# Optimization experiments

Hardware: AMD Instinct MI355X
Metric: run time of the kernel (lower is better)

The kernel has to match this reference:

```python
import jax, jax.numpy as jnp
import numpy as np
from jax import lax

H = W = 224
FH = FW = 7          # backbone feature map spatial size
THRESH = 0.7
NUM_CLASSES = 14


def _conv(x, w, stride, pad):
    return lax.conv_general_dilated(
        x, w, (stride, stride), [(pad, pad), (pad, pad)],
        dimension_numbers=('NCHW', 'OIHW', 'NCHW'))


def backbone(x, w0, w1, w2, w3, fw, fb):
    # stand-in resnet50 trunk: 224 -> 56 -> 28 -> 14 -> 7, channels 3->64->512->1024->2048
    h = jax.nn.relu(_conv(x, w0, 4, 3))      # [B,64,56,56]
    h = jax.nn.relu(_conv(h, w1, 2, 1))      # [B,512,28,28]
    h = jax.nn.relu(_conv(h, w2, 2, 1))      # [B,1024,14,14]
    feat = jax.nn.relu(_conv(h, w3, 2, 1))   # [B,2048,7,7]
    pool = feat.max(axis=(2, 3))             # MaxPool2d(k=7,s=1) on 7x7 == global max -> [B,2048]
    out = jax.nn.sigmoid(pool @ fw.T + fb)   # fc + Sigmoid -> [B,14]
    return out, feat, pool


def attention_gen_patchs(img, fm):
    B, C, Hh, Ww = img.shape
    # per-sample channel-max abs heatmap, min-max normalized
    hm = jnp.max(jnp.abs(fm), axis=1)                              # [B,7,7]
    mn = hm.min(axis=(1, 2), keepdims=True)
    mx = hm.max(axis=(1, 2), keepdims=True)
    hm = (hm - mn) / (mx - mn)
    hm = jax.image.resize(hm, (B, Hh, Ww), method='bilinear')      # Resize((h,w))
    mask = (hm > THRESH).astype(jnp.int32)                         # [B,H,W]

    # largest 8-connected component: iterative max-label propagation
    ids = jnp.arange(1, Hh * Ww + 1, dtype=jnp.int32).reshape(1, Hh, Ww) * mask
    def body(_, lab):
        p = lax.reduce_window(lab, jnp.int32(0), lax.max, (1, 3, 3), (1, 1, 1), 'SAME')
        return p * mask
    labels = lax.fori_loop(0, Hh + Ww, body, ids)                  # [B,H,W] int32

    def counts_one(lab):
        c = jnp.zeros((Hh * Ww + 1,), jnp.int32).at[lab.reshape(-1)].add(1)
        return c.at[0].set(-1)                                     # ignore background
    counts = jax.vmap(counts_one)(labels)                          # [B,H*W+1]
    max_label = jnp.argmax(counts, axis=1)                         # [B]
    lcc = labels == max_label[:, None, None]                       # [B,H,W] bool

    # bbox of largest component (xmin/xmax over rows, ymin/ymax over cols)
    ri = jnp.arange(Hh); ci = jnp.arange(Ww)
    rows = lcc.any(axis=2); cols = lcc.any(axis=1)
    xmin = jnp.min(jnp.where(rows, ri[None, :], Hh), axis=1)
    xmax = jnp.max(jnp.where(rows, ri[None, :], -1), axis=1)       # inclusive; torch slice excludes it
    ymin = jnp.min(jnp.where(cols, ci[None, :], Ww), axis=1)
    ymax = jnp.max(jnp.where(cols, ci[None, :], -1), axis=1)
    ch = jnp.maximum(xmax - xmin, 1).astype(jnp.float32)           # crop height (exclusive slice)
    cw = jnp.maximum(ymax - ymin, 1).astype(jnp.float32)

    # bilinear resize of crop [xmin:xmax, ymin:ymax] back to (H,W), align_corners=False
    fy0 = xmin.astype(jnp.float32); fx0 = ymin.astype(jnp.float32)
    oy = (jnp.arange(Hh, dtype=jnp.float32) + 0.5)[None, :] * (ch[:, None] / Hh) + fy0[:, None] - 0.5
    ox = (jnp.arange(Ww, dtype=jnp.float32) + 0.5)[None, :] * (cw[:, None] / Ww) + fx0[:, None] - 0.5
    oy = jnp.clip(oy, fy0[:, None], jnp.maximum(fy0 + ch - 1.0, fy0)[:, None])
    ox = jnp.clip(ox, fx0[:, None], jnp.maximum(fx0 + cw - 1.0, fx0)[:, None])

    def sample_one(im, yy, xx):  # im [C,H,W]
        gy = jnp.broadcast_to(yy[:, None], (Hh, Ww))
        gx = jnp.broadcast_to(xx[None, :], (Hh, Ww))
        f = lambda chan: jax.scipy.ndimage.map_coordinates(chan, [gy, gx], order=1, mode='nearest')
        return jax.vmap(f)(im)
    return jax.vmap(sample_one)(img, oy, ox)                       # [B,C,H,W]


def bce(p, t):
    p = jnp.clip(p, 1e-7, 1.0 - 1e-7)
    return -jnp.mean(t * jnp.log(p) + (1.0 - t) * jnp.log1p(-p))


def setup_inputs() -> dict:
    key = jax.random.key(0)
    ks = jax.random.split(key, 20)
    B = 4
    def conv_w(k, o, i, s):
        return jax.random.normal(k, (o, i, s, s), jnp.float32) * np.sqrt(2.0 / (i * s * s)).astype(np.float32)
    def lin(k, o, i):
        return jax.random.normal(k, (o, i), jnp.float32) * np.sqrt(1.0 / i).astype(np.float32)
    inp = {
        'img': jax.random.uniform(ks[0], (B, 3, H, W), jnp.float32),
        'target': jax.random.uniform(ks[1], (B, NUM_CLASSES), jnp.float32),
        'gw0': conv_w(ks[2], 64, 3, 7), 'gw1': conv_w(ks[3], 512, 64, 3),
        'gw2': conv_w(ks[4], 1024, 512, 3), 'gw3': conv_w(ks[5], 2048, 1024, 3),
        'gfw': lin(ks[6], NUM_CLASSES, 2048), 'gfb': jnp.zeros((NUM_CLASSES,), jnp.float32),
        'lw0': conv_w(ks[7], 64, 3, 7), 'lw1': conv_w(ks[8], 512, 64, 3),
        'lw2': conv_w(ks[9], 1024, 512, 3), 'lw3': conv_w(ks[10], 2048, 1024, 3),
        'lfw': lin(ks[11], NUM_CLASSES, 2048), 'lfb': jnp.zeros((NUM_CLASSES,), jnp.float32),
        'fw': lin(ks[12], NUM_CLASSES, 2048 * 2), 'fb': jnp.zeros((NUM_CLASSES,), jnp.float32),
    }
    return inp


def reference(img, target, gw0, gw1, gw2, gw3, gfw, gfb,
              lw0, lw1, lw2, lw3, lfw, lfb, fw, fb):
    out_g, fm_g, pool_g = backbone(img, gw0, gw1, gw2, gw3, gfw, gfb)
    # patch generation is non-differentiable in the original (CPU/PIL round trip)
    patch = attention_gen_patchs(lax.stop_gradient(img), lax.stop_gradient(fm_g))
    out_l, _, pool_l = backbone(patch, lw0, lw1, lw2, lw3, lfw, lfb)
    out_f = jax.nn.sigmoid(jnp.concatenate([pool_g, pool_l], axis=1) @ fw.T + fb)
    gl = bce(out_g, target); ll = bce(out_l, target); fl = bce(out_f, target)
    loss = 0.8 * gl + 0.1 * ll + 0.1 * fl
    return loss, out_g, out_l, out_f, patch
```

## Files before the change

kernel.cpp:

```cpp
#include <hip/hip_runtime.h>
#include <math.h>

typedef __attribute__((ext_vector_type(8))) short short8m;
typedef __attribute__((ext_vector_type(4))) float f32x4;

__device__ inline unsigned short bf16_trunc(float f) {
  return (unsigned short)(__float_as_uint(f) >> 16);
}
__device__ inline unsigned short bf16_rte(float f) {
  unsigned u = __float_as_uint(f);
  u += 0x7fffu + ((u >> 16) & 1u);
  return (unsigned short)(u >> 16);
}
__device__ inline float bf16_tof(unsigned short h) {
  return __uint_as_float(((unsigned)h) << 16);
}
__device__ inline short8m* ldsPtr(unsigned short* base, int row, int byteInRow) {
  int off = (row * 128 + byteInRow) ^ ((row & 7) << 4);
  return (short8m*)((char*)base + off);
}
__device__ inline void gload16_lds(const void* g, void* d) {
  __builtin_amdgcn_global_load_lds((const __attribute__((address_space(1))) unsigned int*)g,
                                   (__attribute__((address_space(3))) unsigned int*)d, 16, 0, 0);
}

__global__ __launch_bounds__(256) void k_conv7(const float* __restrict__ x,
                                               const float* __restrict__ w,
                                               float* __restrict__ y) {
  __shared__ float ws[147];
  const int boc = blockIdx.y;
  const int oc = boc & 63;
  const int b = boc >> 6;
  for (int i = threadIdx.x; i < 147; i += 256) ws[i] = w[oc * 147 + i];
  __syncthreads();
  int px = blockIdx.x * 256 + threadIdx.x;
  if (px >= 56 * 56) return;
  int oy = px / 56, ox = px % 56;
  int iy0 = oy * 4 - 3, ix0 = ox * 4 - 3;
  float acc = 0.f;
  for (int c = 0; c < 3; ++c) {
    const float* xp = x + ((size_t)(b * 3 + c)) * 224 * 224;
    #pragma unroll
    for (int ky = 0; ky < 7; ++ky) {
      int iy = iy0 + ky;
      if ((unsigned)iy < 224u) {
        #pragma unroll
        for (int kx = 0; kx < 7; ++kx) {
          int ix = ix0 + kx;
          if ((unsigned)ix < 224u)
            acc += xp[iy * 224 + ix] * ws[c * 49 + ky * 7 + kx];
        }
      }
    }
  }
  y[((size_t)boc * 56 + oy) * 56 + ox] = fmaxf(acc, 0.f);
}

__global__ __launch_bounds__(256) void k_padw(const float* __restrict__ w,
                                              float* __restrict__ wp,
                                              int kreal, int ktot, int noc) {
  int i = blockIdx.x * 256 + threadIdx.x;
  if (i >= noc * ktot) return;
  int oc = i / ktot, k = i % ktot;
  wp[i] = (k < kreal) ? w[oc * kreal + k] : 0.f;
}

template <int CIN, int HIN, int WIN, int HOUT, int WOUT, int KH, int KW, int STR, int PAD, int KTOT>
__global__ __launch_bounds__(256) void k_im2col(const float* __restrict__ x,
                                                unsigned short* __restrict__ XgH,
                                                unsigned short* __restrict__ XgM) {
  constexpr int NPX = 4 * HOUT * WOUT;
  constexpr int K8 = KTOT / 8;
  constexpr int KK = KH * KW;
  int u = blockIdx.x * 256 + threadIdx.x;
  int pxin = u & 63;
  int k8 = (u >> 6) % K8;
  int pxblk = (u >> 6) / K8;
  int px = pxblk * 64 + pxin;
  if (px > NPX - 1) px = NPX - 1;
  const int hw = HOUT * WOUT;
  int pbv = px / hw;
  int r = px % hw;
  int py = r / WOUT, pxv = r % WOUT;
  short8m ph, pm;
  #pragma unroll
  for (int i = 0; i < 8; ++i) {
    int k = k8 * 8 + i;
    int ci = k / KK, tap = k - ci * KK;
    float v = 0.f;
    if (ci < CIN) {
      int iy = py * STR - PAD + tap / KW, ix = pxv * STR - PAD + (tap % KW);
      if ((unsigned)iy < (unsigned)HIN && (unsigned)ix < (unsigned)WIN)
        v = x[(((size_t)pbv * CIN + ci) * HIN + iy) * WIN + ix];
    }
    unsigned short hb = bf16_trunc(v);
    unsigned short mb = bf16_rte(v - bf16_tof(hb));
    ph[i] = (short)hb; pm[i] = (short)mb;
  }
  size_t off = (size_t)u * 8;
  *(short8m*)(XgH + off) = ph;
  *(short8m*)(XgM + off) = pm;
}

template <int COUT, int HOUT, int WOUT, int KTOT, int SPLIT, int OCT>
__global__ __launch_bounds__(OCT * 4) void k_gemmx(const unsigned short* __restrict__ XgH,
                                                   const unsigned short* __restrict__ XgM,
                                                   const float* __restrict__ wsrc,
                                                   float* __restrict__ part) {
  constexpr int NPX = 4 * HOUT * WOUT;
  constexpr int NPXB = (NPX + 63) / 64;
  constexpr int NOCB = COUT / OCT;
  constexpr int NWG = NPXB * NOCB * SPLIT;
  constexpr int KCH = KTOT / SPLIT;
  constexpr int NCH = KCH / 64;
  constexpr int NTHR = OCT * 4;
  constexpr int SLABS = 256 / OCT;
  __shared__ __align__(16) unsigned short XsH[4096];
  __shared__ __align__(16) unsigned short XsM[4096];
  __shared__ __align__(16) unsigned short WsH[OCT * 64];
  __shared__ __align__(16) unsigned short WsM[OCT * 64];
  __shared__ int pb[64], pyA[64], pxA[64];
  const int tid = threadIdx.x;
  const int flat = blockIdx.x;
  constexpr int q = NWG >> 3, r = NWG & 7;
  const int xc = flat & 7, of = flat >> 3;
  const int work = ((xc < r) ? xc * (q + 1) : r * (q + 1) + (xc - r) * q) + of;
  const int pxblk = work % NPXB;
  const int t2 = work / NPXB;
  const int oc0 = (t2 % NOCB) * OCT;
  const int spl = t2 / NOCB;
  if (tid < 64) {
    int p = pxblk * 64 + tid;
    if (p > NPX - 1) p = NPX - 1;
    int hw = HOUT * WOUT;
    pb[tid] = p / hw;
    int rr = p % hw;
    pyA[tid] = rr / WOUT;
    pxA[tid] = rr % WOUT;
  }
  f32x4 acc[4] = {};
  const int l = tid & 63, wv = tid >> 6;
  const int lr = l & 15, lh = l >> 4;
  __syncthreads();
  for (int ch = 0; ch < NCH; ++ch) {
    const int kbase = spl * KCH + ch * 64;
    const size_t tileOff = (size_t)pxblk * KTOT * 64 + (size_t)kbase * 64;
    #pragma unroll
    for (int t = 0; t < SLABS; ++t) {
      int ins = wv * SLABS + t;
      int pl = ins >> 3, ko = ins & 7;
      const unsigned short* g = (pl ? XgM : XgH) + tileOff + ko * 512 + l * 8;
      unsigned short* d = (pl ? XsM : XsH) + ko * 512;
      gload16_lds(g, d);
    }
    #pragma unroll
    for (int j = 0; j < 2; ++j) {
      int c = tid + NTHR * j;
      int oc = c >> 3, koct = c & 7;
      const float* wp = wsrc + (size_t)(oc0 + oc) * KTOT + kbase + koct * 8;
      float vv[8];
      *(float4*)&vv[0] = *(const float4*)wp;
      *(float4*)&vv[4] = *(const float4*)(wp + 4);
      short8m ph, pm;
      #pragma unroll
      for (int i = 0; i < 8; ++i) {
        unsigned short hb = bf16_trunc(vv[i]);
        unsigned short mb = bf16_rte(vv[i] - bf16_tof(hb));
        ph[i] = (short)hb; pm[i] = (short)mb;
      }
      *ldsPtr(WsH, oc, koct * 16) = ph;
      *ldsPtr(WsM, oc, koct * 16) = pm;
    }
    __syncthreads();
    #pragma unroll
    for (int ks = 0; ks < 2; ++ks) {
      const int kbyte = ks * 64 + lh * 16;
      short8m aH = *ldsPtr(WsH, wv * 16 + lr, kbyte);
      short8m aM = *ldsPtr(WsM, wv * 16 + lr, kbyte);
      const int xoff = (ks * 4 + lh) * 512;
      #pragma unroll
      for (int g4 = 0; g4 < 4; ++g4) {
        short8m bH = *(const short8m*)(XsH + xoff + (g4 * 16 + lr) * 8);
        short8m bM = *(const short8m*)(XsM + xoff + (g4 * 16 + lr) * 8);
        acc[g4] = __builtin_amdgcn_mfma_f32_16x16x32_bf16(aH, bH, acc[g4], 0, 0, 0);
        acc[g4] = __builtin_amdgcn_mfma_f32_16x16x32_bf16(aH, bM, acc[g4], 0, 0, 0);
        acc[g4] = __builtin_amdgcn_mfma_f32_16x16x32_bf16(aM, bH, acc[g4], 0, 0, 0);
      }
    }
    __syncthreads();
  }
  const size_t N = (size_t)4 * COUT * HOUT * WOUT;
  #pragma unroll
  for (int g4 = 0; g4 < 4; ++g4) {
    int pxl = g4 * 16 + lr;
    int pidx = pxblk * 64 + pxl;
    if (pidx < NPX) {
      #pragma unroll
      for (int rr = 0; rr < 4; ++rr) {
        int ocl = wv * 16 + lh * 4 + rr;
        float v = acc[g4][rr];
        if (SPLIT == 1) v = fmaxf(v, 0.f);
        part[(size_t)spl * N +
             (((size_t)pb[pxl] * COUT + (oc0 + ocl)) * HOUT + pyA[pxl]) * WOUT + pxA[pxl]] = v;
      }
    }
  }
}

template <int SPLIT>
__global__ __launch_bounds__(256) void k_red(const float* __restrict__ part,
                                             float* __restrict__ y, int n) {
  for (int i = blockIdx.x * 256 + threadIdx.x; i < n; i += gridDim.x * 256) {
    float s = 0.f;
    #pragma unroll
    for (int sp = 0; sp < SPLIT; ++sp) s += part[(size_t)sp * n + i];
    y[i] = fmaxf(s, 0.f);
  }
}

__global__ __launch_bounds__(256) void k_pool(const float* __restrict__ feat,
                                              float* __restrict__ pool) {
  int idx = blockIdx.x * 256 + threadIdx.x;
  if (idx >= 8192) return;
  const float* fp = feat + (size_t)idx * 49;
  float m = fp[0];
  #pragma unroll
  for (int i = 1; i < 49; ++i) m = fmaxf(m, fp[i]);
  pool[idx] = m;
}

__global__ __launch_bounds__(256) void k_fcsig(const float* __restrict__ pool,
                                               const float* __restrict__ fw,
                                               const float* __restrict__ fb,
                                               float* __restrict__ outp) {
  __shared__ float red[256];
  const int blk = blockIdx.x;
  const int b = blk / 14, c = blk % 14;
  const int tid = threadIdx.x;
  float s = 0.f;
  for (int k = tid; k < 2048; k += 256) s += pool[b * 2048 + k] * fw[c * 2048 + k];
  red[tid] = s;
  __syncthreads();
  for (int st = 128; st > 0; st >>= 1) {
    if (tid < st) red[tid] += red[tid + st];
    __syncthreads();
  }
  if (tid == 0) outp[b * 14 + c] = 1.f / (1.f + expf(-(red[0] + fb[c])));
}

__global__ __launch_bounds__(256) void k_fcsig2(const float* __restrict__ poolg,
                                                const float* __restrict__ pooll,
                                                const float* __restrict__ fw,
                                                const float* __restrict__ fb,
                                                float* __restrict__ outp) {
  __shared__ float red[256];
  const int blk = blockIdx.x;
  const int b = blk / 14, c = blk % 14;
  const int tid = threadIdx.x;
  const float* w = fw + (size_t)c * 4096;
  float s = 0.f;
  for (int k = tid; k < 2048; k += 256) s += poolg[b * 2048 + k] * w[k];
  for (int k = tid; k < 2048; k += 256) s += pooll[b * 2048 + k] * w[2048 + k];
  red[tid] = s;
  __syncthreads();
  for (int st = 128; st > 0; st >>= 1) {
    if (tid < st) red[tid] += red[tid + st];
    __syncthreads();
  }
  if (tid == 0) outp[blk] = 1.f / (1.f + expf(-(red[0] + fb[c])));
}

__global__ __launch_bounds__(64) void k_loss(const float* __restrict__ target,
                                             float* __restrict__ dout) {
  __shared__ float red[64];
  const int tid = threadIdx.x;
  float term = 0.f;
  if (tid < 56) {
    float t = target[tid];
    float pg = dout[1 + tid], plo = dout[57 + tid], pf = dout[113 + tid];
    auto bce1 = [&](float pp) {
      pp = fminf(fmaxf(pp, 1e-7f), 1.f - 1e-7f);
      return -(t * logf(pp) + (1.f - t) * log1pf(-pp));
    };
    term = (0.8f * bce1(pg) + 0.1f * bce1(plo) + 0.1f * bce1(pf)) * (1.f / 56.f);
  }
  red[tid] = term;
  __syncthreads();
  for (int st = 32; st > 0; st >>= 1) {
    if (tid < st) red[tid] += red[tid + st];
    __syncthreads();
  }
  if (tid == 0) dout[0] = red[0];
}

__global__ __launch_bounds__(256) void k_hm7a(const float* __restrict__ feat,
                                              float* __restrict__ hmr) {
  __shared__ float red[256];
  const int b = blockIdx.x / 49, cell = blockIdx.x % 49;
  const int tid = threadIdx.x;
  float m = 0.f;
  for (int ch = tid; ch < 2048; ch += 256)
    m = fmaxf(m, fabsf(feat[((size_t)b * 2048 + ch) * 49 + cell]));
  red[tid] = m;
  __syncthreads();
  for (int st = 128; st > 0; st >>= 1) {
    if (tid < st) red[tid] = fmaxf(red[tid], red[tid + st]);
    __syncthreads();
  }
  if (tid == 0) hmr[b * 49 + cell] = red[0];
}

__global__ __launch_bounds__(64) void k_hm7b(const float* __restrict__ hmr,
                                             float* __restrict__ hm7) {
  __shared__ float h[49];
  const int b = blockIdx.x, tid = threadIdx.x;
  if (tid < 49) h[tid] = hmr[b * 49 + tid];
  __syncthreads();
  if (tid == 0) {
    float mn = h[0], mx = h[0];
    for (int i = 1; i < 49; ++i) {
      mn = fminf(mn, h[i]);
      mx = fmaxf(mx, h[i]);
    }
    for (int i = 0; i < 49; ++i) hm7[b * 49 + i] = (h[i] - mn) / (mx - mn);
  }
}

#define MAXR 8
#define NRUNS (224 * MAXR)
#define CTH 1024
__global__ __launch_bounds__(CTH) void k_ccl(const float* __restrict__ hm7, float* __restrict__ bbox) {
  const int b = blockIdx.x, tid = threadIdx.x;
  __shared__ float h7[49];
  __shared__ short rx0[NRUNS], rx1[NRUNS];
  __shared__ short nr[224];
  __shared__ int lab[NRUNS];
  __shared__ int cnt[NRUNS], mid[NRUNS];
  __shared__ int rmn[NRUNS], rmx[NRUNS], cmn[NRUNS], cmx[NRUNS];
  __shared__ int chg;
  __shared__ int bestC[CTH], bestM[CTH], bestI[CTH];

  if (tid < 49) h7[tid] = hm7[b * 49 + tid];
  for (int i = tid; i < NRUNS; i += CTH) {
    cnt[i] = 0; mid[i] = -1;
    rmn[i] = 1 << 30; rmx[i] = -1; cmn[i] = 1 << 30; cmx[i] = -1;
    lab[i] = i;
  }
  __syncthreads();
  if (tid < 224) {
    int yy = tid;
    float py = ((float)yy + 0.5f) * (7.f / 224.f) - 0.5f;
    py = fminf(fmaxf(py, 0.f), 6.f);
    int y0 = (int)floorf(py);
    if (y0 > 5) y0 = 5;
    float fy = py - (float)y0;
    int n = 0, start = -1;
    const int segLo[6] = {0, 48, 80, 112, 144, 176};
    const int segHi[6] = {48, 80, 112, 144, 176, 224};
    #pragma unroll
    for (int s = 0; s < 6; ++s) {
      float A = h7[y0 * 7 + s], B = h7[y0 * 7 + s + 1];
      float C = h7[(y0 + 1) * 7 + s], D = h7[(y0 + 1) * 7 + s + 1];
      for (int xx = segLo[s]; xx < segHi[s]; ++xx) {
        float px = ((float)xx + 0.5f) * (7.f / 224.f) - 0.5f;
        px = fminf(fmaxf(px, 0.f), 6.f);
        float fx = px - (float)s;
        float v = (1.f - fy) * ((1.f - fx) * A + fx * B) +
                  fy * ((1.f - fx) * C + fx * D);
        bool m = v > 0.7f;
        if (m && start < 0) start = xx;
        if (!m && start >= 0) {
          if (n < MAXR) { rx0[yy * MAXR + n] = (short)start; rx1[yy * MAXR + n] = (short)(xx - 1); n++; }
          start = -1;
        }
      }
    }
    if (start >= 0 && n < MAXR) { rx0[yy * MAXR + n] = (short)start; rx1[yy * MAXR + n] = 223; n++; }
    nr[yy] = (short)n;
  }
  __syncthreads();
  int myA0[2], myA1[2];
  bool myV[2];
  #pragma unroll
  for (int j = 0; j < 2; ++j) {
    int i = tid + j * CTH;
    bool v = (i < NRUNS) && ((i & 7) < (int)nr[i >> 3]);
    myV[j] = v;
    myA0[j] = v ? (int)rx0[i] : 0;
    myA1[j] = v ? (int)rx1[i] : 0;
  }
  for (int outer = 0; outer < 128; ++outer) {
    if (tid == 0) chg = 0;
    __syncthreads();
    bool any = false;
    #pragma unroll
    for (int j = 0; j < 2; ++j) {
      if (!myV[j]) continue;
      int i = tid + j * CTH;
      int yy = i >> 3;
      int a0 = myA0[j], a1 = myA1[j];
      int ri = lab[i];
      if (yy > 0) {
        int n1 = nr[yy - 1];
        for (int kk = 0; kk < n1; ++kk) {
          int q = ((yy - 1) << 3) + kk;
          if (a0 <= rx1[q] + 1 && a1 >= rx0[q] - 1) {
            int rq = lab[q];
            if (rq < ri) { atomicMin(&lab[ri], rq); any = true; }
            else if (ri < rq) { atomicMin(&lab[rq], ri); any = true; }
          }
        }
      }
      if (yy < 223) {
        int n1 = nr[yy + 1];
        for (int kk = 0; kk < n1; ++kk) {
          int q = ((yy + 1) << 3) + kk;
          if (a0 <= rx1[q] + 1 && a1 >= rx0[q] - 1) {
            int rq = lab[q];
            if (rq < ri) { atomicMin(&lab[ri], rq); any = true; }
            else if (ri < rq) { atomicMin(&lab[rq], ri); any = true; }
          }
        }
      }
    }
    if (any) chg = 1;
    #pragma unroll
    for (int sc = 0; sc < 3; ++sc) {
      #pragma unroll
      for (int j = 0; j < 2; ++j) {
        int i = tid + j * CTH;
        if (i < NRUNS) {
          int ll = lab[i];
          int l2 = lab[ll];
          if (l2 < ll) lab[i] = l2;
        }
      }
    }
    __syncthreads();
    if (!chg) break;
  }
  for (int i = tid; i < NRUNS; i += CTH) {
    int yy = i >> 3, k = i & 7;
    if (k >= (int)nr[yy]) continue;
    int r = lab[i];
    int a0 = rx0[i], a1 = rx1[i];
    atomicAdd(&cnt[r], a1 - a0 + 1);
    atomicMax(&mid[r], yy * 224 + a1 + 1);
    atomicMin(&rmn[r], yy);
    atomicMax(&rmx[r], yy);
    atomicMin(&cmn[r], a0);
    atomicMax(&cmx[r], a1);
  }
  __syncthreads();
  int bc = -1, bm = 0x7fffffff, bi = -1;
  for (int i = tid; i < NRUNS; i += CTH) {
    if (cnt[i] > 0 && lab[i] == i) {
      if (cnt[i] > bc || (cnt[i] == bc && mid[i] < bm)) { bc = cnt[i]; bm = mid[i]; bi = i; }
    }
  }
  bestC[tid] = bc; bestM[tid] = bm; bestI[tid] = bi;
  __syncthreads();
  for (int st = CTH / 2; st > 0; st >>= 1) {
    if (tid < st) {
      if (bestC[tid + st] > bestC[tid] ||
          (bestC[tid + st] == bestC[tid] && bestM[tid + st] < bestM[tid])) {
        bestC[tid] = bestC[tid + st]; bestM[tid] = bestM[tid + st]; bestI[tid] = bestI[tid + st];
      }
    }
    __syncthreads();
  }
  if (tid == 0) {
    int bw = bestI[0];
    float fy0, chf, fx0, cwf;
    if (bw < 0) { fy0 = 224.f; chf = 1.f; fx0 = 224.f; cwf = 1.f; }
    else {
      int dr = rmx[bw] - rmn[bw]; if (dr < 1) dr = 1;
      int dc = cmx[bw] - cmn[bw]; if (dc < 1) dc = 1;
      fy0 = (float)rmn[bw]; chf = (float)dr;
      fx0 = (float)cmn[bw]; cwf = (float)dc;
    }
    bbox[b * 4 + 0] = fy0; bbox[b * 4 + 1] = chf;
    bbox[b * 4 + 2] = fx0; bbox[b * 4 + 3] = cwf;
  }
}

__global__ __launch_bounds__(256) void k_sample(const float* __restrict__ img,
                                                const float* __restrict__ bbox,
                                                float* __restrict__ patch_out) {
  int idx = blockIdx.x * 256 + threadIdx.x;
  if (idx >= 4 * 3 * 224 * 224) return;
  int b = idx / (3 * 224 * 224);
  int r = idx % (3 * 224 * 224);
  int c = r / (224 * 224);
  int p = r % (224 * 224);
  int oy = p / 224, ox = p % 224;
  float fy0 = bbox[b * 4 + 0], chf = bbox[b * 4 + 1];
  float fx0 = bbox[b * 4 + 2], cwf = bbox[b * 4 + 3];
  float gy = ((float)oy + 0.5f) * (chf / 224.f) + fy0 - 0.5f;
  float gx = ((float)ox + 0.5f) * (cwf / 224.f) + fx0 - 0.5f;
  gy = fminf(fmaxf(gy, fy0), fmaxf(fy0 + chf - 1.f, fy0));
  gx = fminf(fmaxf(gx, fx0), fmaxf(fx0 + cwf - 1.f, fx0));
  int y0 = (int)floorf(gy);
  int x0 = (int)floorf(gx);
  float fy = gy - (float)y0, fx = gx - (float)x0;
  int y0c = min(max(y0, 0), 223), y1c = min(max(y0 + 1, 0), 223);
  int x0c = min(max(x0, 0), 223), x1c = min(max(x0 + 1, 0), 223);
  const float* ip = img + ((size_t)b * 3 + c) * 224 * 224;
  float v00 = ip[y0c * 224 + x0c], v01 = ip[y0c * 224 + x1c];
  float v10 = ip[y1c * 224 + x0c], v11 = ip[y1c * 224 + x1c];
  float v = (1.f - fy) * ((1.f - fx) * v00 + fx * v01) + fy * ((1.f - fx) * v10 + fx * v11);
  patch_out[idx] = v;
}

template <int CIN, int HIN, int WIN, int COUT, int HOUT, int WOUT, int SPLIT>
__global__ __launch_bounds__(256) void k_convm(const float* __restrict__ x,
                                               const float* __restrict__ wsrc,
                                               float* __restrict__ part) {
  constexpr int NPX = 4 * HOUT * WOUT;
  constexpr int KTOT = (CIN * 9) / SPLIT;
  constexpr int NCH = KTOT / 64;
  __shared__ __align__(16) unsigned short Xs[2][64][64];
  __shared__ __align__(16) unsigned short Wsh[3][64][64];
  __shared__ int pb[64], pyA[64], pxA[64];
  const int tid = threadIdx.x;
  const int oc0 = blockIdx.y * 64, px0 = blockIdx.x * 64;
  const int spl = blockIdx.z;
  const int kg0 = spl * KTOT;
  if (tid < 64) {
    int p = px0 + tid;
    if (p > NPX - 1) p = NPX - 1;
    int hw = HOUT * WOUT;
    pb[tid] = p / hw;
    int r = p % hw;
    pyA[tid] = r / WOUT;
    pxA[tid] = r % WOUT;
  }
  f32x4 acc[4] = {};
  const int l = tid & 63, wv = tid >> 6;
  const int lr = l & 15, lh = l >> 4;
  __syncthreads();
  for (int ch = 0; ch < NCH; ++ch) {
    const int kbase = kg0 + ch * 64;
    #pragma unroll
    for (int j = 0; j < 2; ++j) {
      int c = tid + 256 * j;
      int oc = c >> 3, koct = c & 7;
      const float* wp = wsrc + (size_t)(oc0 + oc) * (CIN * 9) + kbase + koct * 8;
      float vv[8];
      *(float4*)&vv[0] = *(const float4*)wp;
      *(float4*)&vv[4] = *(const float4*)(wp + 4);
      short8m ph, pm, pl2;
      #pragma unroll
      for (int i = 0; i < 8; ++i) {
        unsigned short hb = bf16_trunc(vv[i]);
        float r = vv[i] - bf16_tof(hb);
        unsigned short mb = bf16_rte(r);
        float r2 = r - bf16_tof(mb);
        unsigned short lb = bf16_rte(r2);
        ph[i] = (short)hb; pm[i] = (short)mb; pl2[i] = (short)lb;
      }
      *ldsPtr(&Wsh[0][0][0], oc, koct * 16) = ph;
      *ldsPtr(&Wsh[1][0][0], oc, koct * 16) = pm;
      *ldsPtr(&Wsh[2][0][0], oc, koct * 16) = pl2;
    }
    #pragma unroll
    for (int j = 0; j < 2; ++j) {
      int c = tid + 256 * j;
      int px = c & 63, koct = c >> 6;
      int pbv = pb[px], py = pyA[px], pxv = pxA[px];
      float vv[8];
      #pragma unroll
      for (int i = 0; i < 8; ++i) {
        int k = kbase + koct * 8 + i;
        int ci = k / 9, tap = k - ci * 9;
        int iy = py * 2 - 1 + tap / 3, ix = pxv * 2 - 1 + (tap % 3);
        float v = 0.f;
        if ((unsigned)iy < (unsigned)HIN && (unsigned)ix < (unsigned)WIN)
          v = x[(((size_t)pbv * CIN + ci) * HIN + iy) * WIN + ix];
        vv[i] = v;
      }
      short8m ph, pm;
      #pragma unroll
      for (int i = 0; i < 8; ++i) {
        unsigned short hb = bf16_trunc(vv[i]);
        unsigned short mb = bf16_rte(vv[i] - bf16_tof(hb));
        ph[i] = (short)hb; pm[i] = (short)mb;
      }
      *ldsPtr(&Xs[0][0][0], px, koct * 16) = ph;
      *ldsPtr(&Xs[1][0][0], px, koct * 16) = pm;
    }
    __syncthreads();
    #pragma unroll
    for (int ks = 0; ks < 2; ++ks) {
      const int kbyte = ks * 64 + lh * 16;
      short8m aH = *ldsPtr(&Wsh[0][0][0], wv * 16 + lr, kbyte);
      short8m aM = *ldsPtr(&Wsh[1][0][0], wv * 16 + lr, kbyte);
      short8m aL = *ldsPtr(&Wsh[2][0][0], wv * 16 + lr, kbyte);
      #pragma unroll
      for (int g = 0; g < 4; ++g) {
        short8m bH = *ldsPtr(&Xs[0][0][0], g * 16 + lr, kbyte);
        short8m bM = *ldsPtr(&Xs[1][0][0], g * 16 + lr, kbyte);
        acc[g] = __builtin_amdgcn_mfma_f32_16x16x32_bf16(aH, bH, acc[g], 0, 0, 0);
        acc[g] = __builtin_amdgcn_mfma_f32_16x16x32_bf16(aH, bM, acc[g], 0, 0, 0);
        acc[g] = __builtin_amdgcn_mfma_f32_16x16x32_bf16(aM, bH, acc[g], 0, 0, 0);
        acc[g] = __builtin_amdgcn_mfma_f32_16x16x32_bf16(aM, bM, acc[g], 0, 0, 0);
        acc[g] = __builtin_amdgcn_mfma_f32_16x16x32_bf16(aL, bH, acc[g], 0, 0, 0);
      }
    }
    __syncthreads();
  }
  const size_t N = (size_t)4 * COUT * HOUT * WOUT;
  #pragma unroll
  for (int g = 0; g < 4; ++g) {
    int pxl = g * 16 + lr;
    int pidx = px0 + pxl;
    if (pidx < NPX) {
      #pragma unroll
      for (int r = 0; r < 4; ++r) {
        int ocl = wv * 16 + lh * 4 + r;
        part[(size_t)spl * N +
             (((size_t)pb[pxl] * COUT + (oc0 + ocl)) * HOUT + pyA[pxl]) * WOUT + pxA[pxl]] =
            acc[g][r];
      }
    }
  }
}

extern "C" void kernel_launch(void* const* d_in, const int* in_sizes, int n_in,
                              void* d_out, int out_size, void* d_ws, size_t ws_size,
                              hipStream_t stream) {
  const float* img = (const float*)d_in[0];
  const float* target = (const float*)d_in[1];
  const float* gw0 = (const float*)d_in[2];
  const float* gw1 = (const float*)d_in[3];
  const float* gw2 = (const float*)d_in[4];
  const float* gw3 = (const float*)d_in[5];
  const float* gfw = (const float*)d_in[6];
  const float* gfb = (const float*)d_in[7];
  const float* lw0 = (const float*)d_in[8];
  const float* lw1 = (const float*)d_in[9];
  const float* lw2 = (const float*)d_in[10];
  const float* lw3 = (const float*)d_in[11];
  const float* lfw = (const float*)d_in[12];
  const float* lfb = (const float*)d_in[13];
  const float* fw = (const float*)d_in[14];
  const float* fb = (const float*)d_in[15];
  float* out = (float*)d_out;
  float* ws = (float*)d_ws;

  float* c1 = ws;
  float* c2 = c1 + 802816;
  float* c3 = c2 + 1605632;
  float* c4 = c3 + 802816;
  float* poolg = c4 + 401408;
  float* pooll = poolg + 8192;
  float* hm7 = pooll + 8192;
  float* hmr = hm7 + 196;
  float* bbox = hmr + 196;
  float* patch = ws + 3629568;
  float* part = ws + 4231680;
  float* Wp = part + 2800000;
  unsigned short* XgH = (unsigned short*)(ws + 7442944);
  unsigned short* XgM = XgH + 3840000;

  const bool fast = ws_size >= (size_t)45131776;

  dim3 g7(13, 256);
  const int rg2 = 2048, rg3 = 2048, rg4 = 1568;

  for (int pass = 0; pass < 2; ++pass) {
    const float* w0 = pass ? lw0 : gw0;
    const float* w1 = pass ? lw1 : gw1;
    const float* w2 = pass ? lw2 : gw2;
    const float* w3 = pass ? lw3 : gw3;
    const float* fwp = pass ? lfw : gfw;
    const float* fbp = pass ? lfb : gfb;
    const float* inp = pass ? (fast ? (out + 169) : patch) : img;
    float* pool = pass ? pooll : poolg;
    float* outp = pass ? (out + 57) : (out + 1);

    if (fast) {
      k_padw<<<48, 256, 0, stream>>>(w0, Wp, 147, 192, 64);
      k_im2col<3, 224, 224, 56, 56, 7, 7, 4, 3, 192><<<1176, 256, 0, stream>>>(inp, XgH, XgM);
      k_gemmx<64, 56, 56, 192, 1, 64><<<196, 256, 0, stream>>>(XgH, XgM, Wp, c1);
      k_im2col<64, 56, 56, 28, 28, 3, 3, 2, 1, 576><<<882, 256, 0, stream>>>(c1, XgH, XgM);
      k_gemmx<512, 28, 28, 576, 1, 128><<<196, 512, 0, stream>>>(XgH, XgM, w1, c2);
      k_im2col<512, 28, 28, 14, 14, 3, 3, 2, 1, 4608><<<1872, 256, 0, stream>>>(c2, XgH, XgM);
      k_gemmx<1024, 14, 14, 4608, 4, 128><<<416, 512, 0, stream>>>(XgH, XgM, w2, part);
      k_red<4><<<rg3, 256, 0, stream>>>(part, c3, 802816);
      k_im2col<1024, 14, 14, 7, 7, 3, 3, 2, 1, 9216><<<1152, 256, 0, stream>>>(c3, XgH, XgM);
      k_gemmx<2048, 7, 7, 9216, 8, 128><<<512, 512, 0, stream>>>(XgH, XgM, w3, part);
      k_red<8><<<rg4, 256, 0, stream>>>(part, c4, 401408);
    } else {
      k_conv7<<<g7, 256, 0, stream>>>(inp, w0, c1);
      k_convm<64, 56, 56, 512, 28, 28, 1><<<dim3(49, 8, 1), 256, 0, stream>>>(c1, w1, part);
      k_red<1><<<rg2, 256, 0, stream>>>(part, c2, 1605632);
      k_convm<512, 28, 28, 1024, 14, 14, 4><<<dim3(13, 16, 4), 256, 0, stream>>>(c2, w2, part);
      k_red<4><<<rg3, 256, 0, stream>>>(part, c3, 802816);
      k_convm<1024, 14, 14, 2048, 7, 7, 8><<<dim3(4, 32, 8), 256, 0, stream>>>(c3, w3, part);
      k_red<8><<<rg4, 256, 0, stream>>>(part, c4, 401408);
    }
    k_pool<<<32, 256, 0, stream>>>(c4, pool);
    k_fcsig<<<56, 256, 0, stream>>>(pool, fwp, fbp, outp);

    if (pass == 0) {
      k_hm7a<<<196, 256, 0, stream>>>(c4, hmr);
      k_hm7b<<<4, 64, 0, stream>>>(hmr, hm7);
      k_ccl<<<4, CTH, 0, stream>>>(hm7, bbox);
      if (fast) {
        k_sample<<<2352, 256, 0, stream>>>(img, bbox, out + 169);
      } else {
        k_sample<<<2352, 256, 0, stream>>>(img, bbox, out + 169);
        k_sample<<<2352, 256, 0, stream>>>(img, bbox, patch);
      }
    }
  }
  k_fcsig2<<<56, 256, 0, stream>>>(poolg, pooll, fw, fb, out + 113);
  k_loss<<<1, 64, 0, stream>>>(target, out);
}
```

Baseline: 334.2 us.

## Widen GEMM pixel tile to 128 and double split-K for deep conv layers

Parameterizes the im2col and MFMA GEMM kernels by pixel-tile width and, when the workspace is large enough, runs conv3 and conv4 with 128-pixel tiles and twice the split-K factor. Wider pixel tiles reuse each converted weight tile across more pixels, which roughly halves the per-pixel weight fp32-to-bf16 conversion and loading. Doubling the split count keeps the workgroup count up. The cost is larger split-K partial buffers and more reduction traffic, plus a new workspace layout that depends on workspace size. Whether this path runs depends on the harness workspace size.

```diff
diff --git a/kernel.cpp b/kernel.cpp
--- a/kernel.cpp
+++ b/kernel.cpp
@@ -65,7 +65,8 @@
   wp[i] = (k < kreal) ? w[oc * kreal + k] : 0.f;
 }
 
-template <int CIN, int HIN, int WIN, int HOUT, int WOUT, int KH, int KW, int STR, int PAD, int KTOT>
+template <int CIN, int HIN, int WIN, int HOUT, int WOUT, int KH, int KW, int STR, int PAD,
+          int KTOT, int PXT>
 __global__ __launch_bounds__(256) void k_im2col(const float* __restrict__ x,
                                                 unsigned short* __restrict__ XgH,
                                                 unsigned short* __restrict__ XgM) {
@@ -73,10 +74,11 @@
   constexpr int K8 = KTOT / 8;
   constexpr int KK = KH * KW;
   int u = blockIdx.x * 256 + threadIdx.x;
-  int pxin = u & 63;
-  int k8 = (u >> 6) % K8;
-  int pxblk = (u >> 6) / K8;
-  int px = pxblk * 64 + pxin;
+  int pxin = u % PXT;
+  int rest = u / PXT;
+  int k8 = rest % K8;
+  int pxblk = rest / K8;
+  int px = pxblk * PXT + pxin;
   if (px > NPX - 1) px = NPX - 1;
   const int hw = HOUT * WOUT;
   int pbv = px / hw;
@@ -102,24 +104,28 @@
   *(short8m*)(XgM + off) = pm;
 }
 
-template <int COUT, int HOUT, int WOUT, int KTOT, int SPLIT, int OCT>
-__global__ __launch_bounds__(OCT * 4) void k_gemmx(const unsigned short* __restrict__ XgH,
-                                                   const unsigned short* __restrict__ XgM,
-                                                   const float* __restrict__ wsrc,
-                                                   float* __restrict__ part) {
+template <int COUT, int HOUT, int WOUT, int KTOT, int SPLIT, int OCT, int PXT>
+__global__ __launch_bounds__(OCT * 4) void k_gemm(const unsigned short* __restrict__ XgH,
+                                                  const unsigned short* __restrict__ XgM,
+                                                  const float* __restrict__ wsrc,
+                                                  float* __restrict__ part) {
   constexpr int NPX = 4 * HOUT * WOUT;
-  constexpr int NPXB = (NPX + 63) / 64;
+  constexpr int NPXB = (NPX + PXT - 1) / PXT;
   constexpr int NOCB = COUT / OCT;
   constexpr int NWG = NPXB * NOCB * SPLIT;
   constexpr int KCH = KTOT / SPLIT;
   constexpr int NCH = KCH / 64;
   constexpr int NTHR = OCT * 4;
-  constexpr int SLABS = 256 / OCT;
-  __shared__ __align__(16) unsigned short XsH[4096];
-  __shared__ __align__(16) unsigned short XsM[4096];
+  constexpr int NWAVE = NTHR / 64;
+  constexpr int NG = PXT / 16;
+  constexpr int SPP = PXT / 64;
+  constexpr int TS = 16 * SPP;
+  constexpr int SLABSW = TS / NWAVE;
+  __shared__ __align__(16) unsigned short XsH[PXT * 64];
+  __shared__ __align__(16) unsigned short XsM[PXT * 64];
   __shared__ __align__(16) unsigned short WsH[OCT * 64];
   __shared__ __align__(16) unsigned short WsM[OCT * 64];
-  __shared__ int pb[64], pyA[64], pxA[64];
+  __shared__ int pb[PXT], pyA[PXT], pxA[PXT];
   const int tid = threadIdx.x;
   const int flat = blockIdx.x;
   constexpr int q = NWG >> 3, r = NWG & 7;
@@ -129,8 +135,8 @@
   const int t2 = work / NPXB;
   const int oc0 = (t2 % NOCB) * OCT;
   const int spl = t2 / NOCB;
-  if (tid < 64) {
-    int p = pxblk * 64 + tid;
+  if (tid < PXT) {
+    int p = pxblk * PXT + tid;
     if (p > NPX - 1) p = NPX - 1;
     int hw = HOUT * WOUT;
     pb[tid] = p / hw;
@@ -138,19 +144,22 @@
     pyA[tid] = rr / WOUT;
     pxA[tid] = rr % WOUT;
   }
-  f32x4 acc[4] = {};
+  f32x4 acc[NG] = {};
   const int l = tid & 63, wv = tid >> 6;
   const int lr = l & 15, lh = l >> 4;
   __syncthreads();
   for (int ch = 0; ch < NCH; ++ch) {
     const int kbase = spl * KCH + ch * 64;
-    const size_t tileOff = (size_t)pxblk * KTOT * 64 + (size_t)kbase * 64;
-    #pragma unroll
-    for (int t = 0; t < SLABS; ++t) {
-      int ins = wv * SLABS + t;
-      int pl = ins >> 3, ko = ins & 7;
-      const unsigned short* g = (pl ? XgM : XgH) + tileOff + ko * 512 + l * 8;
-      unsigned short* d = (pl ? XsM : XsH) + ko * 512;
+    const size_t tileOff = (size_t)pxblk * KTOT * PXT + (size_t)kbase * PXT;
+    #pragma unroll
+    for (int t = 0; t < SLABSW; ++t) {
+      int ins = wv * SLABSW + t;
+      int pl = ins >= (TS / 2);
+      int wp = ins - pl * (TS / 2);
+      int ko = wp / SPP, sp = wp % SPP;
+      const unsigned short* g =
+          (pl ? XgM : XgH) + tileOff + (size_t)ko * (PXT * 8) + sp * 512 + l * 8;
+      unsigned short* d = (pl ? XsM : XsH) + ko * (PXT * 8) + sp * 512;
       gload16_lds(g, d);
     }
     #pragma unroll
@@ -177,9 +186,9 @@
       const int kbyte = ks * 64 + lh * 16;
       short8m aH = *ldsPtr(WsH, wv * 16 + lr, kbyte);
       short8m aM = *ldsPtr(WsM, wv * 16 + lr, kbyte);
-      const int xoff = (ks * 4 + lh) * 512;
-      #pragma unroll
-      for (int g4 = 0; g4 < 4; ++g4) {
+      const int xoff = (ks * 4 + lh) * (PXT * 8);
+      #pragma unroll
+      for (int g4 = 0; g4 < NG; ++g4) {
         short8m bH = *(const short8m*)(XsH + xoff + (g4 * 16 + lr) * 8);
         short8m bM = *(const short8m*)(XsM + xoff + (g4 * 16 + lr) * 8);
         acc[g4] = __builtin_amdgcn_mfma_f32_16x16x32_bf16(aH, bH, acc[g4], 0, 0, 0);
@@ -191,9 +200,9 @@
   }
   const size_t N = (size_t)4 * COUT * HOUT * WOUT;
   #pragma unroll
-  for (int g4 = 0; g4 < 4; ++g4) {
+  for (int g4 = 0; g4 < NG; ++g4) {
     int pxl = g4 * 16 + lr;
-    int pidx = pxblk * 64 + pxl;
+    int pidx = pxblk * PXT + pxl;
     if (pidx < NPX) {
       #pragma unroll
       for (int rr = 0; rr < 4; ++rr) {
@@ -658,11 +667,17 @@
   float* hmr = hm7 + 196;
   float* bbox = hmr + 196;
   float* patch = ws + 3629568;
-  float* part = ws + 4231680;
-  float* Wp = part + 2800000;
-  unsigned short* XgH = (unsigned short*)(ws + 7442944);
-  unsigned short* XgM = XgH + 3840000;
-
+
+  float* part1 = ws + 4231680;
+  float* Wp1 = part1 + 2800000;
+  unsigned short* XgH1 = (unsigned short*)(ws + 7442944);
+  unsigned short* XgM1 = XgH1 + 3840000;
+  float* part2 = ws + 4231680;
+  float* Wp2 = part2 + 6300000;
+  unsigned short* XgH2 = (unsigned short*)(ws + 10654208);
+  unsigned short* XgM2 = XgH2 + 4200448;
+
+  const bool tier2 = ws_size >= (size_t)59419648;
   const bool fast = ws_size >= (size_t)45131776;
 
   dim3 g7(13, 256);
@@ -679,19 +694,40 @@
     float* pool = pass ? pooll : poolg;
     float* outp = pass ? (out + 57) : (out + 1);
 
-    if (fast) {
+    if (tier2) {
+      float* part = part2;
+      unsigned short* XgH = XgH2;
+      unsigned short* XgM = XgM2;
+      float* Wp = part2;
       k_padw<<<48, 256, 0, stream>>>(w0, Wp, 147, 192, 64);
-      k_im2col<3, 224, 224, 56, 56, 7, 7, 4, 3, 192><<<1176, 256, 0, stream>>>(inp, XgH, XgM);
-      k_gemmx<64, 56, 56, 192, 1, 64><<<196, 256, 0, stream>>>(XgH, XgM, Wp, c1);
-      k_im2col<64, 56, 56, 28, 28, 3, 3, 2, 1, 576><<<882, 256, 0, stream>>>(c1, XgH, XgM);
-      k_gemmx<512, 28, 28, 576, 1, 128><<<196, 512, 0, stream>>>(XgH, XgM, w1, c2);
-      k_im2col<512, 28, 28, 14, 14, 3, 3, 2, 1, 4608><<<1872, 256, 0, stream>>>(c2, XgH, XgM);
-      k_gemmx<1024, 14, 14, 4608, 4, 128><<<416, 512, 0, stream>>>(XgH, XgM, w2, part);
+      k_im2col<3, 224, 224, 56, 56, 7, 7, 4, 3, 192, 64><<<1176, 256, 0, stream>>>(inp, XgH, XgM);
+      k_gemm<64, 56, 56, 192, 1, 64, 64><<<196, 256, 0, stream>>>(XgH, XgM, Wp, c1);
+      k_im2col<64, 56, 56, 28, 28, 3, 3, 2, 1, 576, 64><<<882, 256, 0, stream>>>(c1, XgH, XgM);
+      k_gemm<512, 28, 28, 576, 1, 128, 64><<<196, 512, 0, stream>>>(XgH, XgM, w1, c2);
+      k_im2col<512, 28, 28, 14, 14, 3, 3, 2, 1, 4608, 128><<<2016, 256, 0, stream>>>(c2, XgH, XgM);
+      k_gemm<1024, 14, 14, 4608, 8, 128, 128><<<448, 512, 0, stream>>>(XgH, XgM, w2, part);
+      k_red<8><<<rg3, 256, 0, stream>>>(part, c3, 802816);
+      k_im2col<1024, 14, 14, 7, 7, 3, 3, 2, 1, 9216, 128><<<1152, 256, 0, stream>>>(c3, XgH, XgM);
+      k_gemm<2048, 7, 7, 9216, 16, 128, 128><<<512, 512, 0, stream>>>(XgH, XgM, w3, part);
+      k_red<16><<<rg4, 256, 0, stream>>>(part, c4, 401408);
+    } else if (fast) {
+      float* part = part1;
+      unsigned short* XgH = XgH1;
+      unsigned short* XgM = XgM1;
+      float* Wp = Wp1;
+      k_padw<<<48, 256, 0, stream>>>(w0, Wp, 147, 192, 64);
+      k_im2col<3, 224, 224, 56, 56, 7, 7, 4, 3, 192, 64><<<1176, 256, 0, stream>>>(inp, XgH, XgM);
+      k_gemm<64, 56, 56, 192, 1, 64, 64><<<196, 256, 0, stream>>>(XgH, XgM, Wp, c1);
+      k_im2col<64, 56, 56, 28, 28, 3, 3, 2, 1, 576, 64><<<882, 256, 0, stream>>>(c1, XgH, XgM);
+      k_gemm<512, 28, 28, 576, 1, 128, 64><<<196, 512, 0, stream>>>(XgH, XgM, w1, c2);
+      k_im2col<512, 28, 28, 14, 14, 3, 3, 2, 1, 4608, 64><<<1872, 256, 0, stream>>>(c2, XgH, XgM);
+      k_gemm<1024, 14, 14, 4608, 4, 128, 64><<<416, 512, 0, stream>>>(XgH, XgM, w2, part);
       k_red<4><<<rg3, 256, 0, stream>>>(part, c3, 802816);
-      k_im2col<1024, 14, 14, 7, 7, 3, 3, 2, 1, 9216><<<1152, 256, 0, stream>>>(c3, XgH, XgM);
-      k_gemmx<2048, 7, 7, 9216, 8, 128><<<512, 512, 0, stream>>>(XgH, XgM, w3, part);
+      k_im2col<1024, 14, 14, 7, 7, 3, 3, 2, 1, 9216, 64><<<1152, 256, 0, stream>>>(c3, XgH, XgM);
+      k_gemm<2048, 7, 7, 9216, 8, 128, 64><<<512, 512, 0, stream>>>(XgH, XgM, w3, part);
       k_red<8><<<rg4, 256, 0, stream>>>(part, c4, 401408);
     } else {
+      float* part = part1;
       k_conv7<<<g7, 256, 0, stream>>>(inp, w0, c1);
       k_convm<64, 56, 56, 512, 28, 28, 1><<<dim3(49, 8, 1), 256, 0, stream>>>(c1, w1, part);
       k_red<1><<<rg2, 256, 0, stream>>>(part, c2, 1605632);
@@ -707,12 +743,8 @@
       k_hm7a<<<196, 256, 0, stream>>>(c4, hmr);
       k_hm7b<<<4, 64, 0, stream>>>(hmr, hm7);
       k_ccl<<<4, CTH, 0, stream>>>(hm7, bbox);
-      if (fast) {
-        k_sample<<<2352, 256, 0, stream>>>(img, bbox, out + 169);
-      } else {
-        k_sample<<<2352, 256, 0, stream>>>(img, bbox, out + 169);
-        k_sample<<<2352, 256, 0, stream>>>(img, bbox, patch);
-      }
+      k_sample<<<2352, 256, 0, stream>>>(img, bbox, out + 169);
+      if (!fast) k_sample<<<2352, 256, 0, stream>>>(img, bbox, patch);
     }
   }
   k_fcsig2<<<56, 256, 0, stream>>>(poolg, pooll, fw, fb, out + 113);
```

After: 330.3 us. About the same (-1.2%).
